# Kernel tuning notes

Hardware: AMD Instinct MI355X
Metric: run time of the kernel (lower is better)

The kernel has to match this reference:

```python
import jax, jax.numpy as jnp
import numpy as np

B, S, D_MODEL, D_Q = 16, 2048, 384, 64


def setup_inputs() -> dict:
    key = jax.random.key(0)
    k1, k2, k3, k4 = jax.random.split(key, 4)
    x = jax.random.normal(k1, (B, S, D_MODEL), dtype=jnp.float32)
    # nn.Linear(d_model, d_q, bias=False) weights, stored as [d_model, d_q] so q = x @ Wq
    scale = 1.0 / np.sqrt(D_MODEL)
    Wq = jax.random.normal(k2, (D_MODEL, D_Q), dtype=jnp.float32) * scale
    Wk = jax.random.normal(k3, (D_MODEL, D_Q), dtype=jnp.float32) * scale
    Wv = jax.random.normal(k4, (D_MODEL, D_Q), dtype=jnp.float32) * scale
    return {"x": x, "Wq": Wq, "Wk": Wk, "Wv": Wv}


def reference(x, Wq, Wk, Wv):
    # x: [B, S, d_model]
    q = jnp.einsum("bsd,de->bse", x, Wq)  # [B, S, d_q]
    k = jnp.einsum("bsd,de->bse", x, Wk)
    v = jnp.einsum("bsd,de->bse", x, Wv)
    d_q = q.shape[-1]
    # full S x S score matrix, scaled by sqrt(d_q) as in the torch code (k.size(-1)**0.5)
    scores = jnp.einsum("bse,bte->bst", q, k) / jnp.sqrt(jnp.float32(d_q))
    s = x.shape[1]
    causal = jnp.tril(jnp.ones((s, s), dtype=bool))  # [S, S]
    scores = jnp.where(causal, scores, jnp.float32(-jnp.inf))
    probs = jax.nn.softmax(scores, axis=-1)
    # dropout is identity in eval/reference mode
    out = jnp.einsum("bst,bte->bse", probs, v)  # [B, S, d_q]
    return out
```

## Files before the change

kernel.cpp:

```cpp
#include <hip/hip_runtime.h>
#include <hip/hip_bf16.h>
#include <math.h>

#define BB 16
#define SS 2048
#define DM 384
#define DQ 64
#define M_ROWS (BB * SS)

typedef short short8 __attribute__((ext_vector_type(8)));
typedef float f32x4  __attribute__((ext_vector_type(4)));
typedef unsigned u32x4 __attribute__((ext_vector_type(4)));

#define WT_OFF 0
#define QB_OFF 73728
#define KB_OFF (QB_OFF + M_ROWS * DQ)
#define VT_OFF (KB_OFF + M_ROWS * DQ)
#define OP_OFF (VT_OFF + BB * DQ * SS)
#define LS_OFF (OP_OFF + 2 * M_ROWS * DQ * 2)

#define QSCALE 0.18033688011112042f

__device__ __forceinline__ short f2bf(float f) {
  unsigned u = __builtin_bit_cast(unsigned, f);
  unsigned r = (u + 0x7fffu + ((u >> 16) & 1u)) >> 16;
  return (short)r;
}
__device__ __forceinline__ unsigned cvtpk(float a, float b) {
  unsigned r;
  asm("v_cvt_pk_bf16_f32 %0, %1, %2" : "=v"(r) : "v"(a), "v"(b));
  return r;
}
__device__ __forceinline__ void async16(const short* g, short* l) {
  __builtin_amdgcn_global_load_lds(
      (const __attribute__((address_space(1))) unsigned int*)g,
      (__attribute__((address_space(3))) unsigned int*)l, 16, 0, 0);
}

__global__ void prep_w_kernel(const float* __restrict__ Wq,
                              const float* __restrict__ Wk,
                              const float* __restrict__ Wv,
                              short* __restrict__ ws) {
  int o = blockIdx.x * 256 + threadIdx.x;
  int mat = o / (DM * DQ);
  int r = o % (DM * DQ);
  int k = r / DQ, n = r % DQ;
  const float* W = (mat == 0) ? Wq : (mat == 1) ? Wk : Wv;
  ws[WT_OFF + mat * (DM * DQ) + n * DM + k] = f2bf(W[k * DQ + n]);
}

__global__ __launch_bounds__(256) void qkv_proj_mfma(
    const float* __restrict__ x, const short* __restrict__ ws_r,
    short* __restrict__ ws_w) {
  __shared__ short smem[2 * 192 * 64];
  short* Ep = smem;
  const int tid = threadIdx.x;
  const int lane = tid & 63, w = tid >> 6;
  const int cidx = lane & 15, g = lane >> 4;
  const int g8 = g * 8, g4 = g * 4;
  const int sw7 = cidx & 7;
  const int rows0 = blockIdx.x * 64;
  const short* Wt = ws_r + WT_OFF;

  f32x4 acc[12];
  #pragma unroll
  for (int i = 0; i < 12; ++i) acc[i] = (f32x4){0.f, 0.f, 0.f, 0.f};

  const float* xr = x + (size_t)(rows0 + 16 * w + cidx) * DM;

  #pragma unroll
  for (int it = 0; it < 6; ++it) {
    int i = it * 256 + tid;
    int row = i >> 3, gr = i & 7;
    const short* src = Wt + row * DM + ((gr ^ (row & 7)) * 8);
    async16(src, &smem[(it * 256 + w * 64) * 8]);
  }
  float4 xc0 = *(const float4*)(xr + g8);
  float4 xc1 = *(const float4*)(xr + g8 + 4);
  float4 xc2 = *(const float4*)(xr + 32 + g8);
  float4 xc3 = *(const float4*)(xr + 32 + g8 + 4);

  for (int ki = 0; ki < 6; ++ki) {
    __syncthreads();
    const short* cur = smem + (ki & 1) * 12288;

    if (ki < 5) {
      short* nxt = smem + ((ki + 1) & 1) * 12288;
      const int kn = (ki + 1) * 64;
      #pragma unroll
      for (int it = 0; it < 6; ++it) {
        int i = it * 256 + tid;
        int row = i >> 3, gr = i & 7;
        const short* src = Wt + row * DM + kn + ((gr ^ (row & 7)) * 8);
        async16(src, &nxt[(it * 256 + w * 64) * 8]);
      }
    }

    u32x4 ua, ub;
    ua[0] = cvtpk(xc0.x, xc0.y); ua[1] = cvtpk(xc0.z, xc0.w);
    ua[2] = cvtpk(xc1.x, xc1.y); ua[3] = cvtpk(xc1.z, xc1.w);
    ub[0] = cvtpk(xc2.x, xc2.y); ub[1] = cvtpk(xc2.z, xc2.w);
    ub[2] = cvtpk(xc3.x, xc3.y); ub[3] = cvtpk(xc3.z, xc3.w);
    short8 a0 = __builtin_bit_cast(short8, ua);
    short8 a1 = __builtin_bit_cast(short8, ub);

    if (ki < 5) {
      const float* xn = xr + (ki + 1) * 64;
      xc0 = *(const float4*)(xn + g8);
      xc1 = *(const float4*)(xn + g8 + 4);
      xc2 = *(const float4*)(xn + 32 + g8);
      xc3 = *(const float4*)(xn + 32 + g8 + 4);
    }

    #pragma unroll
    for (int ct = 0; ct < 12; ++ct) {
      int row = ct * 16 + cidx;
      short8 b0 = *(const short8*)&cur[row * 64 + ((g ^ sw7) * 8)];
      short8 b1 = *(const short8*)&cur[row * 64 + (((g + 4) ^ sw7) * 8)];
      acc[ct] = __builtin_amdgcn_mfma_f32_16x16x32_bf16(a0, b0, acc[ct], 0, 0, 0);
      acc[ct] = __builtin_amdgcn_mfma_f32_16x16x32_bf16(a1, b1, acc[ct], 0, 0, 0);
    }
  }

  __syncthreads();
  const int erow = 16 * w + g4;
  #pragma unroll
  for (int ct = 0; ct < 4; ++ct) {
    unsigned q01 = cvtpk(acc[ct][0] * QSCALE, acc[ct][1] * QSCALE);
    unsigned q23 = cvtpk(acc[ct][2] * QSCALE, acc[ct][3] * QSCALE);
    unsigned k01 = cvtpk(acc[4 + ct][0], acc[4 + ct][1]);
    unsigned k23 = cvtpk(acc[4 + ct][2], acc[4 + ct][3]);
    unsigned v01 = cvtpk(acc[8 + ct][0], acc[8 + ct][1]);
    unsigned v23 = cvtpk(acc[8 + ct][2], acc[8 + ct][3]);
    Ep[(erow + 0) * 200 + ct * 16 + cidx] = (short)q01;
    Ep[(erow + 1) * 200 + ct * 16 + cidx] = (short)(q01 >> 16);
    Ep[(erow + 2) * 200 + ct * 16 + cidx] = (short)q23;
    Ep[(erow + 3) * 200 + ct * 16 + cidx] = (short)(q23 >> 16);
    Ep[(erow + 0) * 200 + 64 + ct * 16 + cidx] = (short)k01;
    Ep[(erow + 1) * 200 + 64 + ct * 16 + cidx] = (short)(k01 >> 16);
    Ep[(erow + 2) * 200 + 64 + ct * 16 + cidx] = (short)k23;
    Ep[(erow + 3) * 200 + 64 + ct * 16 + cidx] = (short)(k23 >> 16);
    Ep[(ct * 16 + cidx) * 200 + 128 + erow + 0] = (short)v01;
    Ep[(ct * 16 + cidx) * 200 + 128 + erow + 1] = (short)(v01 >> 16);
    Ep[(ct * 16 + cidx) * 200 + 128 + erow + 2] = (short)v23;
    Ep[(ct * 16 + cidx) * 200 + 128 + erow + 3] = (short)(v23 >> 16);
  }
  __syncthreads();

  short* Qb = ws_w + QB_OFF;
  short* Kb = ws_w + KB_OFF;
  short* Vt = ws_w + VT_OFF;
  const int bidx = rows0 >> 11;
  const int srow0 = rows0 & 2047;
  #pragma unroll
  for (int t2 = 0; t2 < 2; ++t2) {
    int i = t2 * 256 + tid;
    int row = i >> 3, gq = i & 7;
    *(short8*)&Qb[(size_t)(rows0 + row) * DQ + gq * 8] =
        *(const short8*)&Ep[row * 200 + gq * 8];
    *(short8*)&Kb[(size_t)(rows0 + row) * DQ + gq * 8] =
        *(const short8*)&Ep[row * 200 + 64 + gq * 8];
    *(short8*)&Vt[(size_t)bidx * (64 * SS) + (size_t)row * SS + srow0 + gq * 8] =
        *(const short8*)&Ep[row * 200 + 128 + gq * 8];
  }
}

__global__ __launch_bounds__(256, 4) void flash_mfma(
    const short* __restrict__ ws, float* __restrict__ Op,
    float* __restrict__ Ls) {
  __shared__ short smem[20480];
  const int l = blockIdx.x;
  const int b = l & 15;
  const int r = l >> 4;
  const int qtp = r & 31;
  const int half = r >> 5;
  const int qt = (qtp < 16) ? qtp : 47 - qtp;
  const int q0 = qt * 64;
  const int hsplit = ((qt + 2) >> 1) * 64;
  const int kstart = half ? hsplit : 0;
  const int kend = half ? (qt + 1) * 64 : hsplit;
  const int nss = (kend - kstart) >> 6;

  const int tid = threadIdx.x;
  const int lane = tid & 63, w = tid >> 6;
  const int cidx = lane & 15, g = lane >> 4;
  const int g8 = g * 8, g4 = g * 4;
  const int sw7 = cidx & 7;
  short* Ps = smem + 16384 + w * 1024;

  const short* Qb = ws + QB_OFF + (size_t)b * SS * DQ;
  const short* Kb = ws + KB_OFF + (size_t)b * SS * DQ;
  const short* Vt = ws + VT_OFF + (size_t)b * 64 * SS;

  const int qrow = q0 + w * 16;
  const int qglob = qrow + cidx;
  short8 qf0 = *(const short8*)&Qb[(size_t)qglob * DQ + g8];
  short8 qf1 = *(const short8*)&Qb[(size_t)qglob * DQ + 32 + g8];

  const int srow = tid >> 3, sgr = tid & 7;
  const int ssw = (sgr ^ (srow & 7)) * 8;
  const short* kb0 = Kb + (size_t)(kstart + srow) * DQ + ssw;
  const short* kb1 = Kb + (size_t)(kstart + srow + 32) * DQ + ssw;
  const short* vb0 = Vt + (size_t)srow * SS + kstart + ssw;
  const short* vb1 = Vt + (size_t)(srow + 32) * SS + kstart + ssw;
  const int dst0 = (w * 64) * 8, dst1 = (256 + w * 64) * 8;

  f32x4 o[4];
  #pragma unroll
  for (int i = 0; i < 4; ++i) o[i] = (f32x4){0.f, 0.f, 0.f, 0.f};
  float lsum = 0.f;

  if (nss > 0) {
    async16(kb0, &smem[dst0]);
    async16(kb1, &smem[dst1]);
    async16(vb0, &smem[8192 + dst0]);
    async16(vb1, &smem[8192 + dst1]);

    for (int ssi = 0; ssi < nss; ++ssi) {
      __syncthreads();

      {
        int nb = (ssi + 1) * 64;
        if (nb >= kend - kstart) nb = 0;
        const int nbuf = ((ssi + 1) & 1) * 4096;
        const size_t koff = (size_t)nb * DQ;
        async16(kb0 + koff, &smem[nbuf + dst0]);
        async16(kb1 + koff, &smem[nbuf + dst1]);
        async16(vb0 + nb, &smem[8192 + nbuf + dst0]);
        async16(vb1 + nb, &smem[8192 + nbuf + dst1]);
      }

      const short* Kc = smem + (ssi & 1) * 4096;
      const short* Vc = smem + 8192 + (ssi & 1) * 4096;
      const int kbase = kstart + ssi * 64;

      f32x4 sc[4];
      __builtin_amdgcn_s_setprio(1);
      #pragma unroll
      for (int ct = 0; ct < 4; ++ct) {
        int krow = ct * 16 + cidx;
        short8 kf0 = *(const short8*)&Kc[krow * 64 + ((g ^ sw7) * 8)];
        short8 kf1 = *(const short8*)&Kc[krow * 64 + (((g + 4) ^ sw7) * 8)];
        f32x4 a = (f32x4){0.f, 0.f, 0.f, 0.f};
        a = __builtin_amdgcn_mfma_f32_16x16x32_bf16(kf0, qf0, a, 0, 0, 0);
        a = __builtin_amdgcn_mfma_f32_16x16x32_bf16(kf1, qf1, a, 0, 0, 0);
        sc[ct] = a;
      }
      __builtin_amdgcn_s_setprio(0);
      if (ssi == nss - 1) {
        #pragma unroll
        for (int ct = 0; ct < 4; ++ct) {
          int key = kbase + ct * 16 + g4;
          #pragma unroll
          for (int rr = 0; rr < 4; ++rr)
            if (key + rr > qglob) sc[ct][rr] = -1e30f;
        }
      }
      #pragma unroll
      for (int ct = 0; ct < 4; ++ct) {
        #pragma unroll
        for (int rr = 0; rr < 4; ++rr) {
          float p = __builtin_amdgcn_exp2f(sc[ct][rr]);
          sc[ct][rr] = p;
          lsum += p;
        }
        int gb = ct * 2 + (g >> 1);
        uint2 pk;
        pk.x = cvtpk(sc[ct][0], sc[ct][1]);
        pk.y = cvtpk(sc[ct][2], sc[ct][3]);
        *(uint2*)&Ps[cidx * 64 + ((gb ^ sw7) * 8) + (g & 1) * 4] = pk;
      }
      __builtin_amdgcn_s_setprio(1);
      #pragma unroll
      for (int ks = 0; ks < 2; ++ks) {
        short8 pf = *(const short8*)&Ps[cidx * 64 + (((ks * 4 + g) ^ sw7) * 8)];
        #pragma unroll
        for (int dt = 0; dt < 4; ++dt) {
          int vrow = dt * 16 + cidx;
          short8 vf = *(const short8*)&Vc[vrow * 64 + (((ks * 4 + g) ^ sw7) * 8)];
          o[dt] = __builtin_amdgcn_mfma_f32_16x16x32_bf16(vf, pf, o[dt], 0, 0, 0);
        }
      }
      __builtin_amdgcn_s_setprio(0);
    }
  }

  lsum += __shfl_xor(lsum, 16);
  lsum += __shfl_xor(lsum, 32);

  float* op = Op + (size_t)half * (M_ROWS * DQ) + ((size_t)b * SS + qglob) * DQ;
  #pragma unroll
  for (int dt = 0; dt < 4; ++dt) {
    float4 v = make_float4(o[dt][0], o[dt][1], o[dt][2], o[dt][3]);
    *(float4*)&op[dt * 16 + g4] = v;
  }
  if (g == 0)
    Ls[(size_t)half * M_ROWS + (size_t)b * SS + qglob] = lsum;
}

__global__ __launch_bounds__(256) void norm_kernel(
    const float* __restrict__ Op, const float* __restrict__ Ls,
    float* __restrict__ O) {
  int idx = blockIdx.x * 256 + threadIdx.x;
  int row = idx >> 4, q4 = idx & 15;
  float li = 1.0f / (Ls[row] + Ls[M_ROWS + row]);
  float4 a = *(const float4*)&Op[(size_t)row * DQ + q4 * 4];
  float4 c = *(const float4*)&Op[(size_t)(M_ROWS + row) * DQ + q4 * 4];
  float4 v = make_float4((a.x + c.x) * li, (a.y + c.y) * li,
                         (a.z + c.z) * li, (a.w + c.w) * li);
  *(float4*)&O[(size_t)row * DQ + q4 * 4] = v;
}

extern "C" void kernel_launch(void* const* d_in, const int* in_sizes, int n_in,
                              void* d_out, int out_size, void* d_ws, size_t ws_size,
                              hipStream_t stream) {
  const float* x  = (const float*)d_in[0];
  const float* Wq = (const float*)d_in[1];
  const float* Wk = (const float*)d_in[2];
  const float* Wv = (const float*)d_in[3];
  short* ws = (short*)d_ws;
  float* out = (float*)d_out;
  float* Op = (float*)(ws + OP_OFF);
  float* Ls = (float*)(ws + LS_OFF);

  prep_w_kernel<<<288, 256, 0, stream>>>(Wq, Wk, Wv, ws);
  qkv_proj_mfma<<<M_ROWS / 64, 256, 0, stream>>>(x, ws, ws);
  flash_mfma<<<1024, 256, 0, stream>>>(ws, Op, Ls);
  norm_kernel<<<2048, 256, 0, stream>>>(Op, Ls, out);
}
```

Measured before the change: 123.3 us.

## Load K and V fragments directly from global memory, dropping LDS staging

Removes the double-buffered async global-to-LDS staging of K and V tiles and the per-iteration block barrier. Each wave now reads its MFMA K and V fragments straight from global memory (through the caches), and LDS is used only for the per-wave P tile. This cuts shared memory use and synchronization, which may raise occupancy. In exchange, each of the four waves issues redundant global loads for the same K/V tile and there is no explicit prefetch to hide latency.

```diff
diff --git a/kernel.cpp b/kernel.cpp
--- a/kernel.cpp
+++ b/kernel.cpp
@@ -168,7 +168,7 @@
 __global__ __launch_bounds__(256, 4) void flash_mfma(
     const short* __restrict__ ws, float* __restrict__ Op,
     float* __restrict__ Ls) {
-  __shared__ short smem[20480];
+  __shared__ short Psm[4 * 1024];
   const int l = blockIdx.x;
   const int b = l & 15;
   const int r = l >> 4;
@@ -186,7 +186,7 @@
   const int cidx = lane & 15, g = lane >> 4;
   const int g8 = g * 8, g4 = g * 4;
   const int sw7 = cidx & 7;
-  short* Ps = smem + 16384 + w * 1024;
+  short* Ps = Psm + w * 1024;
 
   const short* Qb = ws + QB_OFF + (size_t)b * SS * DQ;
   const short* Kb = ws + KB_OFF + (size_t)b * SS * DQ;
@@ -197,92 +197,65 @@
   short8 qf0 = *(const short8*)&Qb[(size_t)qglob * DQ + g8];
   short8 qf1 = *(const short8*)&Qb[(size_t)qglob * DQ + 32 + g8];
 
-  const int srow = tid >> 3, sgr = tid & 7;
-  const int ssw = (sgr ^ (srow & 7)) * 8;
-  const short* kb0 = Kb + (size_t)(kstart + srow) * DQ + ssw;
-  const short* kb1 = Kb + (size_t)(kstart + srow + 32) * DQ + ssw;
-  const short* vb0 = Vt + (size_t)srow * SS + kstart + ssw;
-  const short* vb1 = Vt + (size_t)(srow + 32) * SS + kstart + ssw;
-  const int dst0 = (w * 64) * 8, dst1 = (256 + w * 64) * 8;
-
   f32x4 o[4];
   #pragma unroll
   for (int i = 0; i < 4; ++i) o[i] = (f32x4){0.f, 0.f, 0.f, 0.f};
   float lsum = 0.f;
 
-  if (nss > 0) {
-    async16(kb0, &smem[dst0]);
-    async16(kb1, &smem[dst1]);
-    async16(vb0, &smem[8192 + dst0]);
-    async16(vb1, &smem[8192 + dst1]);
-
-    for (int ssi = 0; ssi < nss; ++ssi) {
-      __syncthreads();
-
-      {
-        int nb = (ssi + 1) * 64;
-        if (nb >= kend - kstart) nb = 0;
-        const int nbuf = ((ssi + 1) & 1) * 4096;
-        const size_t koff = (size_t)nb * DQ;
-        async16(kb0 + koff, &smem[nbuf + dst0]);
-        async16(kb1 + koff, &smem[nbuf + dst1]);
-        async16(vb0 + nb, &smem[8192 + nbuf + dst0]);
-        async16(vb1 + nb, &smem[8192 + nbuf + dst1]);
-      }
-
-      const short* Kc = smem + (ssi & 1) * 4096;
-      const short* Vc = smem + 8192 + (ssi & 1) * 4096;
-      const int kbase = kstart + ssi * 64;
-
-      f32x4 sc[4];
-      __builtin_amdgcn_s_setprio(1);
+  const short* kp = Kb + (size_t)(kstart + cidx) * DQ + g8;
+  const short* vp = Vt + (size_t)cidx * SS + kstart + g8;
+
+  for (int ssi = 0; ssi < nss; ++ssi) {
+    const int kbase = kstart + ssi * 64;
+    const short* kc = kp + (size_t)ssi * 64 * DQ;
+
+    f32x4 sc[4];
+    __builtin_amdgcn_s_setprio(1);
+    #pragma unroll
+    for (int ct = 0; ct < 4; ++ct) {
+      short8 kf0 = *(const short8*)&kc[(size_t)ct * 16 * DQ];
+      short8 kf1 = *(const short8*)&kc[(size_t)ct * 16 * DQ + 32];
+      f32x4 a = (f32x4){0.f, 0.f, 0.f, 0.f};
+      a = __builtin_amdgcn_mfma_f32_16x16x32_bf16(kf0, qf0, a, 0, 0, 0);
+      a = __builtin_amdgcn_mfma_f32_16x16x32_bf16(kf1, qf1, a, 0, 0, 0);
+      sc[ct] = a;
+    }
+    __builtin_amdgcn_s_setprio(0);
+    if (ssi == nss - 1) {
       #pragma unroll
       for (int ct = 0; ct < 4; ++ct) {
-        int krow = ct * 16 + cidx;
-        short8 kf0 = *(const short8*)&Kc[krow * 64 + ((g ^ sw7) * 8)];
-        short8 kf1 = *(const short8*)&Kc[krow * 64 + (((g + 4) ^ sw7) * 8)];
-        f32x4 a = (f32x4){0.f, 0.f, 0.f, 0.f};
-        a = __builtin_amdgcn_mfma_f32_16x16x32_bf16(kf0, qf0, a, 0, 0, 0);
-        a = __builtin_amdgcn_mfma_f32_16x16x32_bf16(kf1, qf1, a, 0, 0, 0);
-        sc[ct] = a;
+        int key = kbase + ct * 16 + g4;
+        #pragma unroll
+        for (int rr = 0; rr < 4; ++rr)
+          if (key + rr > qglob) sc[ct][rr] = -1e30f;
       }
-      __builtin_amdgcn_s_setprio(0);
-      if (ssi == nss - 1) {
-        #pragma unroll
-        for (int ct = 0; ct < 4; ++ct) {
-          int key = kbase + ct * 16 + g4;
-          #pragma unroll
-          for (int rr = 0; rr < 4; ++rr)
-            if (key + rr > qglob) sc[ct][rr] = -1e30f;
-        }
+    }
+    #pragma unroll
+    for (int ct = 0; ct < 4; ++ct) {
+      #pragma unroll
+      for (int rr = 0; rr < 4; ++rr) {
+        float p = __builtin_amdgcn_exp2f(sc[ct][rr]);
+        sc[ct][rr] = p;
+        lsum += p;
       }
+      int gb = ct * 2 + (g >> 1);
+      uint2 pk;
+      pk.x = cvtpk(sc[ct][0], sc[ct][1]);
+      pk.y = cvtpk(sc[ct][2], sc[ct][3]);
+      *(uint2*)&Ps[cidx * 64 + ((gb ^ sw7) * 8) + (g & 1) * 4] = pk;
+    }
+    __builtin_amdgcn_s_setprio(1);
+    #pragma unroll
+    for (int ks = 0; ks < 2; ++ks) {
+      short8 pf = *(const short8*)&Ps[cidx * 64 + (((ks * 4 + g) ^ sw7) * 8)];
+      const short* vc = vp + (size_t)ssi * 64 + ks * 32;
       #pragma unroll
-      for (int ct = 0; ct < 4; ++ct) {
-        #pragma unroll
-        for (int rr = 0; rr < 4; ++rr) {
-          float p = __builtin_amdgcn_exp2f(sc[ct][rr]);
-          sc[ct][rr] = p;
-          lsum += p;
-        }
-        int gb = ct * 2 + (g >> 1);
-        uint2 pk;
-        pk.x = cvtpk(sc[ct][0], sc[ct][1]);
-        pk.y = cvtpk(sc[ct][2], sc[ct][3]);
-        *(uint2*)&Ps[cidx * 64 + ((gb ^ sw7) * 8) + (g & 1) * 4] = pk;
+      for (int dt = 0; dt < 4; ++dt) {
+        short8 vf = *(const short8*)&vc[(size_t)dt * 16 * SS];
+        o[dt] = __builtin_amdgcn_mfma_f32_16x16x32_bf16(vf, pf, o[dt], 0, 0, 0);
       }
-      __builtin_amdgcn_s_setprio(1);
-      #pragma unroll
-      for (int ks = 0; ks < 2; ++ks) {
-        short8 pf = *(const short8*)&Ps[cidx * 64 + (((ks * 4 + g) ^ sw7) * 8)];
-        #pragma unroll
-        for (int dt = 0; dt < 4; ++dt) {
-          int vrow = dt * 16 + cidx;
-          short8 vf = *(const short8*)&Vc[vrow * 64 + (((ks * 4 + g) ^ sw7) * 8)];
-          o[dt] = __builtin_amdgcn_mfma_f32_16x16x32_bf16(vf, pf, o[dt], 0, 0, 0);
-        }
-      }
-      __builtin_amdgcn_s_setprio(0);
-    }
+    }
+    __builtin_amdgcn_s_setprio(0);
   }
 
   lsum += __shfl_xor(lsum, 16);
```

Result: slower. 167.6 us (+35.9%).

## Split QKV projection across blocks per matrix with XCD-aware row tiling

Applied to the files above, without the earlier changes.

The QKV projection now launches three times as many blocks, one per (row tile, matrix), and block indices are mapped so that the three matrices for a row tile land on the same XCD and can share x through its L2. Each block loads its whole 64x384 weight slice into LDS once instead of double-buffering across k-steps, and writes results straight from registers without the LDS staging epilogue. This raises parallelism and cuts per-block register and sync cost, but reads x three times from global memory and makes Q/K stores narrow 2-byte scatters.

```diff
diff --git a/kernel.cpp b/kernel.cpp
--- a/kernel.cpp
+++ b/kernel.cpp
@@ -49,53 +49,47 @@
   ws[WT_OFF + mat * (DM * DQ) + n * DM + k] = f2bf(W[k * DQ + n]);
 }
 
-__global__ __launch_bounds__(256) void qkv_proj_mfma(
+__global__ __launch_bounds__(256, 3) void qkv_proj_v2(
     const float* __restrict__ x, const short* __restrict__ ws_r,
     short* __restrict__ ws_w) {
-  __shared__ short smem[2 * 192 * 64];
-  short* Ep = smem;
+  __shared__ short Ws[64 * 384];
   const int tid = threadIdx.x;
   const int lane = tid & 63, w = tid >> 6;
   const int cidx = lane & 15, g = lane >> 4;
   const int g8 = g * 8, g4 = g * 4;
   const int sw7 = cidx & 7;
-  const int rows0 = blockIdx.x * 64;
-  const short* Wt = ws_r + WT_OFF;
-
-  f32x4 acc[12];
+
+  const int l = blockIdx.x;
+  const int xcd = l & 7;
+  const int idx = l >> 3;
+  const int mat = idx % 3;
+  const int rtl = idx / 3;
+  const int rt = rtl * 8 + xcd;
+  const int rows0 = rt * 64;
+
+  const short* Wtg = ws_r + WT_OFF + mat * (DM * DQ);
+
   #pragma unroll
-  for (int i = 0; i < 12; ++i) acc[i] = (f32x4){0.f, 0.f, 0.f, 0.f};
+  for (int it = 0; it < 12; ++it) {
+    int i = it * 256 + tid;
+    int n = i / 48, gr = i % 48;
+    const short* src = Wtg + n * DM + (gr >> 3) * 64 + (((gr & 7) ^ (n & 7)) * 8);
+    async16(src, &Ws[i * 8]);
+  }
 
   const float* xr = x + (size_t)(rows0 + 16 * w + cidx) * DM;
-
-  #pragma unroll
-  for (int it = 0; it < 6; ++it) {
-    int i = it * 256 + tid;
-    int row = i >> 3, gr = i & 7;
-    const short* src = Wt + row * DM + ((gr ^ (row & 7)) * 8);
-    async16(src, &smem[(it * 256 + w * 64) * 8]);
-  }
   float4 xc0 = *(const float4*)(xr + g8);
   float4 xc1 = *(const float4*)(xr + g8 + 4);
   float4 xc2 = *(const float4*)(xr + 32 + g8);
   float4 xc3 = *(const float4*)(xr + 32 + g8 + 4);
 
+  f32x4 acc[4];
+  #pragma unroll
+  for (int i = 0; i < 4; ++i) acc[i] = (f32x4){0.f, 0.f, 0.f, 0.f};
+
+  __syncthreads();
+
   for (int ki = 0; ki < 6; ++ki) {
-    __syncthreads();
-    const short* cur = smem + (ki & 1) * 12288;
-
-    if (ki < 5) {
-      short* nxt = smem + ((ki + 1) & 1) * 12288;
-      const int kn = (ki + 1) * 64;
-      #pragma unroll
-      for (int it = 0; it < 6; ++it) {
-        int i = it * 256 + tid;
-        int row = i >> 3, gr = i & 7;
-        const short* src = Wt + row * DM + kn + ((gr ^ (row & 7)) * 8);
-        async16(src, &nxt[(it * 256 + w * 64) * 8]);
-      }
-    }
-
     u32x4 ua, ub;
     ua[0] = cvtpk(xc0.x, xc0.y); ua[1] = cvtpk(xc0.z, xc0.w);
     ua[2] = cvtpk(xc1.x, xc1.y); ua[3] = cvtpk(xc1.z, xc1.w);
@@ -113,55 +107,38 @@
     }
 
     #pragma unroll
-    for (int ct = 0; ct < 12; ++ct) {
+    for (int ct = 0; ct < 4; ++ct) {
       int row = ct * 16 + cidx;
-      short8 b0 = *(const short8*)&cur[row * 64 + ((g ^ sw7) * 8)];
-      short8 b1 = *(const short8*)&cur[row * 64 + (((g + 4) ^ sw7) * 8)];
+      const short* wrow = &Ws[row * 384 + ki * 64];
+      short8 b0 = *(const short8*)&wrow[(g ^ sw7) * 8];
+      short8 b1 = *(const short8*)&wrow[((g + 4) ^ sw7) * 8];
       acc[ct] = __builtin_amdgcn_mfma_f32_16x16x32_bf16(a0, b0, acc[ct], 0, 0, 0);
       acc[ct] = __builtin_amdgcn_mfma_f32_16x16x32_bf16(a1, b1, acc[ct], 0, 0, 0);
     }
   }
 
-  __syncthreads();
   const int erow = 16 * w + g4;
-  #pragma unroll
-  for (int ct = 0; ct < 4; ++ct) {
-    unsigned q01 = cvtpk(acc[ct][0] * QSCALE, acc[ct][1] * QSCALE);
-    unsigned q23 = cvtpk(acc[ct][2] * QSCALE, acc[ct][3] * QSCALE);
-    unsigned k01 = cvtpk(acc[4 + ct][0], acc[4 + ct][1]);
-    unsigned k23 = cvtpk(acc[4 + ct][2], acc[4 + ct][3]);
-    unsigned v01 = cvtpk(acc[8 + ct][0], acc[8 + ct][1]);
-    unsigned v23 = cvtpk(acc[8 + ct][2], acc[8 + ct][3]);
-    Ep[(erow + 0) * 200 + ct * 16 + cidx] = (short)q01;
-    Ep[(erow + 1) * 200 + ct * 16 + cidx] = (short)(q01 >> 16);
-    Ep[(erow + 2) * 200 + ct * 16 + cidx] = (short)q23;
-    Ep[(erow + 3) * 200 + ct * 16 + cidx] = (short)(q23 >> 16);
-    Ep[(erow + 0) * 200 + 64 + ct * 16 + cidx] = (short)k01;
-    Ep[(erow + 1) * 200 + 64 + ct * 16 + cidx] = (short)(k01 >> 16);
-    Ep[(erow + 2) * 200 + 64 + ct * 16 + cidx] = (short)k23;
-    Ep[(erow + 3) * 200 + 64 + ct * 16 + cidx] = (short)(k23 >> 16);
-    Ep[(ct * 16 + cidx) * 200 + 128 + erow + 0] = (short)v01;
-    Ep[(ct * 16 + cidx) * 200 + 128 + erow + 1] = (short)(v01 >> 16);
-    Ep[(ct * 16 + cidx) * 200 + 128 + erow + 2] = (short)v23;
-    Ep[(ct * 16 + cidx) * 200 + 128 + erow + 3] = (short)(v23 >> 16);
-  }
-  __syncthreads();
-
-  short* Qb = ws_w + QB_OFF;
-  short* Kb = ws_w + KB_OFF;
-  short* Vt = ws_w + VT_OFF;
-  const int bidx = rows0 >> 11;
-  const int srow0 = rows0 & 2047;
-  #pragma unroll
-  for (int t2 = 0; t2 < 2; ++t2) {
-    int i = t2 * 256 + tid;
-    int row = i >> 3, gq = i & 7;
-    *(short8*)&Qb[(size_t)(rows0 + row) * DQ + gq * 8] =
-        *(const short8*)&Ep[row * 200 + gq * 8];
-    *(short8*)&Kb[(size_t)(rows0 + row) * DQ + gq * 8] =
-        *(const short8*)&Ep[row * 200 + 64 + gq * 8];
-    *(short8*)&Vt[(size_t)bidx * (64 * SS) + (size_t)row * SS + srow0 + gq * 8] =
-        *(const short8*)&Ep[row * 200 + 128 + gq * 8];
+  if (mat == 2) {
+    short* Vt = ws_w + VT_OFF;
+    const int bidx = rows0 >> 11;
+    const int srow0 = rows0 & 2047;
+    #pragma unroll
+    for (int ct = 0; ct < 4; ++ct) {
+      uint2 pk;
+      pk.x = cvtpk(acc[ct][0], acc[ct][1]);
+      pk.y = cvtpk(acc[ct][2], acc[ct][3]);
+      *(uint2*)&Vt[(size_t)bidx * (64 * SS) + (size_t)(ct * 16 + cidx) * SS +
+                   srow0 + erow] = pk;
+    }
+  } else {
+    short* Ob = ws_w + (mat == 0 ? QB_OFF : KB_OFF);
+    const float sc = (mat == 0) ? QSCALE : 1.0f;
+    #pragma unroll
+    for (int ct = 0; ct < 4; ++ct)
+      #pragma unroll
+      for (int rr = 0; rr < 4; ++rr)
+        Ob[(size_t)(rows0 + erow + rr) * DQ + ct * 16 + cidx] =
+            f2bf(acc[ct][rr] * sc);
   }
 }
 
@@ -324,7 +301,7 @@
   float* Ls = (float*)(ws + LS_OFF);
 
   prep_w_kernel<<<288, 256, 0, stream>>>(Wq, Wk, Wv, ws);
-  qkv_proj_mfma<<<M_ROWS / 64, 256, 0, stream>>>(x, ws, ws);
+  qkv_proj_v2<<<1536, 256, 0, stream>>>(x, ws, ws);
   flash_mfma<<<1024, 256, 0, stream>>>(ws, Op, Ls);
   norm_kernel<<<2048, 256, 0, stream>>>(Op, Ls, out);
 }
```

After: 130.3 us. 5.7% more time.
